# Optimization experiments

Hardware: AMD Instinct MI355X
Metric: run time of the kernel (lower is better)

Reference implementation:

```python
import jax, jax.numpy as jnp
import numpy as np

UNITS = 14336
IN_FEATURES = 4096
PACKED = IN_FEATURES // 4  # 4 ternary values (2 bits each) per byte
CLIP_VAL = 100.0

# 2-bit crumb -> ternary value lookup: 0 -> 0, 1 -> +1, 2 -> -1, 3 -> 0
_TERNARY_LUT = jnp.array([0.0, 1.0, -1.0, 0.0], dtype=jnp.float32)


def _unpack_ternary(pw):
    """pw: [U, P] int (byte values 0..255) -> dense ternary float W [U, 4*P].
    Little-endian crumbs within each byte (shifts 0,2,4,6)."""
    crumbs = jnp.stack([(pw >> (2 * i)) & 3 for i in range(4)], axis=-1)  # [U, P, 4]
    crumbs = crumbs.reshape(pw.shape[0], -1)  # [U, 4*P]
    return _TERNARY_LUT[crumbs][:, :IN_FEATURES]  # [U, IN]


def setup_inputs() -> dict:
    key = jax.random.key(0)
    k1, k2, k3, k4 = jax.random.split(key, 4)
    x = jax.random.normal(k1, (32, IN_FEATURES), dtype=jnp.float32)
    # packed ternary weights, one uint8-valued byte per 4 ternary weights
    pw = jax.random.randint(k2, (UNITS, PACKED), 0, 256, dtype=jnp.int32)
    scale = 1.0 + 0.02 * jax.random.normal(k3, (UNITS,), dtype=jnp.float32)
    bias = 0.01 * jax.random.normal(k4, (UNITS,), dtype=jnp.float32)
    return {"x": x, "pw": pw, "scale": scale, "bias": bias}


def reference(x, pw, scale, bias):
    # dense ternary weight [UNITS, IN]; kernel target would fuse this unpack into the GEMM
    W = _unpack_ternary(pw)
    y = jnp.einsum('bd,ud->bu', x, W)  # [B, UNITS]
    y = y * scale + bias               # per-unit affine dequant
    return jnp.clip(y, -CLIP_VAL, CLIP_VAL)
```

## Files before the change

### kernel.cpp

```cpp
#include <hip/hip_runtime.h>

#define UNITS 14336
#define IN_F 4096
#define PACKED 1024
#define CLIP_VAL 100.0f

typedef unsigned int uint32;

using bf16x8 = __attribute__((ext_vector_type(8))) short;
using f32x4  = __attribute__((ext_vector_type(4))) float;

__device__ uint4 g_xw[16384];

__device__ inline unsigned short f2bf(float f) {
    uint32 u = __float_as_uint(f);
    u += 0x7FFFu + ((u >> 16) & 1u);
    return (unsigned short)(u >> 16);
}

__device__ inline uint32 pack2bf(float a, float b) {
    return (uint32)f2bf(a) | ((uint32)f2bf(b) << 16);
}

__device__ inline void unpack_byte(int v, uint32& r0, uint32& r1) {
    uint32 t0 = ((uint32)v & 3u) | (((uint32)v & 0xCu) << 14);
    uint32 t1 = (((uint32)v >> 4) & 3u) | (((uint32)v & 0xC0u) << 10);
    uint32 s0 = t0 >> 1;
    uint32 s1 = t1 >> 1;
    uint32 nz0 = (t0 ^ s0) & 0x00010001u;
    uint32 nz1 = (t1 ^ s1) & 0x00010001u;
    r0 = nz0 * 0x3F80u + ((s0 & 0x00010001u) << 15);
    r1 = nz1 * 0x3F80u + ((s1 & 0x00010001u) << 15);
}

__device__ inline float clipf(float y) {
    return fminf(fmaxf(y, -CLIP_VAL), CLIP_VAL);
}


__global__ __launch_bounds__(256) void convert_x_kernel(
    const float* __restrict__ x) {
    int t = blockIdx.x * 256 + threadIdx.x;
    int lane = t & 63;
    int h = (t >> 6) & 1;
    int s = (t >> 7) & 1;
    int g = t >> 8;
    int n = lane & 15;
    int q = lane >> 4;
    int b = h * 16 + n;
    int k0 = g * 64 + q * 16 + s * 8;
    const float4* src = (const float4*)(x + (size_t)b * IN_F + k0);
    float4 lo = src[0];
    float4 hi = src[1];
    uint4 o;
    o.x = pack2bf(lo.x, lo.y);
    o.y = pack2bf(lo.z, lo.w);
    o.z = pack2bf(hi.x, hi.y);
    o.w = pack2bf(hi.z, hi.w);
    g_xw[t] = o;
}

__global__ __launch_bounds__(1024, 8) void ternary_mm_kernel(
    const int*   __restrict__ pw,
    const float* __restrict__ scale,
    const float* __restrict__ bias,
    float*       __restrict__ out) {
    __shared__ int lds4[16640];
    char* lds = (char*)lds4;

    const int tid  = threadIdx.x;
    const int wid  = tid >> 6;
    const int lane = tid & 63;
    const int q    = lane >> 4;
    const int n    = lane & 15;
    const int u0   = blockIdx.x << 4;
    const int g0   = wid << 2;

    {
        const char* src = (const char*)(pw + (size_t)u0 * PACKED);
        #pragma unroll
        for (int j = 0; j < 4; ++j) {
            const int Rs = j * 16 + wid;
            __builtin_amdgcn_global_load_lds(
                (const __attribute__((address_space(1))) uint32*)
                    (src + (Rs << 10) + (lane << 4)),
                (__attribute__((address_space(3))) uint32*)
                    (lds + Rs * 1040),
                16, 0, 0);
        }
    }

    const uint4* xb = g_xw + (g0 << 8) + lane;
    uint4 xa0 = xb[0], xa1 = xb[64], xa2 = xb[128], xa3 = xb[192];

    __syncthreads();

    f32x4 acc0 = {0.f,0.f,0.f,0.f};
    f32x4 acc1 = {0.f,0.f,0.f,0.f};

    const int R = (n << 2) + (wid >> 2);
    const char* lb = lds + R * 1040 + ((wid & 3) << 8) + (q << 4);

    #pragma unroll
    for (int i = 0; i < 4; ++i) {
        uint4 xn0, xn1, xn2, xn3;
        if (i < 3) {
            const uint4* xi = xb + ((i + 1) << 8);
            xn0 = xi[0]; xn1 = xi[64]; xn2 = xi[128]; xn3 = xi[192];
        }
        int4 w4 = *(const int4*)(lb + (i << 6));

        uint4 fA, fB;
        unpack_byte(w4.x, fA.x, fA.y);
        unpack_byte(w4.y, fA.z, fA.w);
        unpack_byte(w4.z, fB.x, fB.y);
        unpack_byte(w4.w, fB.z, fB.w);
        bf16x8 vA = __builtin_bit_cast(bf16x8, fA);
        bf16x8 vB = __builtin_bit_cast(bf16x8, fB);

        acc0 = __builtin_amdgcn_mfma_f32_16x16x32_bf16(
            __builtin_bit_cast(bf16x8, xa0), vA, acc0, 0, 0, 0);
        acc1 = __builtin_amdgcn_mfma_f32_16x16x32_bf16(
            __builtin_bit_cast(bf16x8, xa1), vA, acc1, 0, 0, 0);
        acc0 = __builtin_amdgcn_mfma_f32_16x16x32_bf16(
            __builtin_bit_cast(bf16x8, xa2), vB, acc0, 0, 0, 0);
        acc1 = __builtin_amdgcn_mfma_f32_16x16x32_bf16(
            __builtin_bit_cast(bf16x8, xa3), vB, acc1, 0, 0, 0);

        if (i < 3) { xa0 = xn0; xa1 = xn1; xa2 = xn2; xa3 = xn3; }
    }

    __syncthreads();
    f32x4* red = (f32x4*)lds;
    red[(wid * 2 + 0) * 64 + lane] = acc0;
    red[(wid * 2 + 1) * 64 + lane] = acc1;
    __syncthreads();

    if (tid < 128) {
        const int h = tid >> 6;
        const int l = tid & 63;
        f32x4 s = red[h * 64 + l];
        #pragma unroll
        for (int w = 1; w < 16; ++w) {
            f32x4 v = red[(w * 2 + h) * 64 + l];
            s[0] += v[0]; s[1] += v[1]; s[2] += v[2]; s[3] += v[3];
        }
        const int u  = u0 + (l & 15);
        const int b0 = h * 16 + ((l >> 4) << 2);
        const float sc = scale[u];
        const float bi = bias[u];
        float* o = out + (size_t)b0 * UNITS + u;
        o[0 * UNITS] = clipf(s[0] * sc + bi);
        o[1 * UNITS] = clipf(s[1] * sc + bi);
        o[2 * UNITS] = clipf(s[2] * sc + bi);
        o[3 * UNITS] = clipf(s[3] * sc + bi);
    }
}

extern "C" void kernel_launch(void* const* d_in, const int* in_sizes, int n_in,
                              void* d_out, int out_size, void* d_ws, size_t ws_size,
                              hipStream_t stream) {
    const float* x     = (const float*)d_in[0];
    const int*   pw    = (const int*)d_in[1];
    const float* scale = (const float*)d_in[2];
    const float* bias  = (const float*)d_in[3];
    float* out = (float*)d_out;

    (void)d_ws; (void)ws_size;

    convert_x_kernel<<<64, 256, 0, stream>>>(x);
    ternary_mm_kernel<<<UNITS / 16, 1024, 0, stream>>>(pw, scale, bias, out);
}
```

Measured before the change: 103.9 us.

## Fuse x bf16 conversion into ternary GEMM and halve block size

Removes the separate convert_x kernel and its global bf16 staging buffer, so each block now loads fp32 x directly and converts it to bf16 in registers before the MFMAs. The block shrinks from 16 to 8 waves, each covering twice the K range with an 8-iteration loop, and the cross-wave reduction drops to 8 partials. This saves one kernel launch and the round trip through global memory, but every block now reads fp32 x (twice the bytes of bf16) and redoes the conversion, which adds redundant ALU and L2 traffic across all 896 blocks.

```diff
diff --git a/kernel.cpp b/kernel.cpp
--- a/kernel.cpp
+++ b/kernel.cpp
@@ -1,4 +1,5 @@
 #include <hip/hip_runtime.h>
+#include <hip/hip_bf16.h>
 
 #define UNITS 14336
 #define IN_F 4096
@@ -10,16 +11,10 @@
 using bf16x8 = __attribute__((ext_vector_type(8))) short;
 using f32x4  = __attribute__((ext_vector_type(4))) float;
 
-__device__ uint4 g_xw[16384];
-
-__device__ inline unsigned short f2bf(float f) {
-    uint32 u = __float_as_uint(f);
-    u += 0x7FFFu + ((u >> 16) & 1u);
-    return (unsigned short)(u >> 16);
-}
-
 __device__ inline uint32 pack2bf(float a, float b) {
-    return (uint32)f2bf(a) | ((uint32)f2bf(b) << 16);
+    unsigned short lo = __builtin_bit_cast(unsigned short, __float2bfloat16(a));
+    unsigned short hi = __builtin_bit_cast(unsigned short, __float2bfloat16(b));
+    return (uint32)lo | ((uint32)hi << 16);
 }
 
 __device__ inline void unpack_byte(int v, uint32& r0, uint32& r1) {
@@ -37,30 +32,8 @@
     return fminf(fmaxf(y, -CLIP_VAL), CLIP_VAL);
 }
 
-
-__global__ __launch_bounds__(256) void convert_x_kernel(
-    const float* __restrict__ x) {
-    int t = blockIdx.x * 256 + threadIdx.x;
-    int lane = t & 63;
-    int h = (t >> 6) & 1;
-    int s = (t >> 7) & 1;
-    int g = t >> 8;
-    int n = lane & 15;
-    int q = lane >> 4;
-    int b = h * 16 + n;
-    int k0 = g * 64 + q * 16 + s * 8;
-    const float4* src = (const float4*)(x + (size_t)b * IN_F + k0);
-    float4 lo = src[0];
-    float4 hi = src[1];
-    uint4 o;
-    o.x = pack2bf(lo.x, lo.y);
-    o.y = pack2bf(lo.z, lo.w);
-    o.z = pack2bf(hi.x, hi.y);
-    o.w = pack2bf(hi.z, hi.w);
-    g_xw[t] = o;
-}
-
-__global__ __launch_bounds__(1024, 8) void ternary_mm_kernel(
+__global__ __launch_bounds__(512, 4) void ternary_mm_fused(
+    const float* __restrict__ x,
     const int*   __restrict__ pw,
     const float* __restrict__ scale,
     const float* __restrict__ bias,
@@ -74,13 +47,12 @@
     const int q    = lane >> 4;
     const int n    = lane & 15;
     const int u0   = blockIdx.x << 4;
-    const int g0   = wid << 2;
 
     {
         const char* src = (const char*)(pw + (size_t)u0 * PACKED);
         #pragma unroll
-        for (int j = 0; j < 4; ++j) {
-            const int Rs = j * 16 + wid;
+        for (int j = 0; j < 8; ++j) {
+            const int Rs = j * 8 + wid;
             __builtin_amdgcn_global_load_lds(
                 (const __attribute__((address_space(1))) uint32*)
                     (src + (Rs << 10) + (lane << 4)),
@@ -90,24 +62,44 @@
         }
     }
 
-    const uint4* xb = g_xw + (g0 << 8) + lane;
-    uint4 xa0 = xb[0], xa1 = xb[64], xa2 = xb[128], xa3 = xb[192];
+    const float* xp0 = x + (size_t)n * IN_F + (wid << 9) + (q << 4);
+    const float* xp1 = xp0 + (size_t)16 * IN_F;
+
+    float4 a0, a1, a2, a3, b0, b1, b2, b3;
+    {
+        const float4* p0 = (const float4*)xp0;
+        const float4* p1 = (const float4*)xp1;
+        a0 = p0[0]; a1 = p0[1]; a2 = p0[2]; a3 = p0[3];
+        b0 = p1[0]; b1 = p1[1]; b2 = p1[2]; b3 = p1[3];
+    }
 
     __syncthreads();
 
     f32x4 acc0 = {0.f,0.f,0.f,0.f};
     f32x4 acc1 = {0.f,0.f,0.f,0.f};
 
-    const int R = (n << 2) + (wid >> 2);
-    const char* lb = lds + R * 1040 + ((wid & 3) << 8) + (q << 4);
+    const int R = (n << 2) + (wid >> 1);
+    const char* lb = lds + R * 1040 + ((wid & 1) << 9) + (q << 4);
 
     #pragma unroll
-    for (int i = 0; i < 4; ++i) {
-        uint4 xn0, xn1, xn2, xn3;
-        if (i < 3) {
-            const uint4* xi = xb + ((i + 1) << 8);
-            xn0 = xi[0]; xn1 = xi[64]; xn2 = xi[128]; xn3 = xi[192];
+    for (int i = 0; i < 8; ++i) {
+        uint4 xa0, xa1, xa2, xa3;
+        xa0.x = pack2bf(a0.x, a0.y); xa0.y = pack2bf(a0.z, a0.w);
+        xa0.z = pack2bf(a1.x, a1.y); xa0.w = pack2bf(a1.z, a1.w);
+        xa2.x = pack2bf(a2.x, a2.y); xa2.y = pack2bf(a2.z, a2.w);
+        xa2.z = pack2bf(a3.x, a3.y); xa2.w = pack2bf(a3.z, a3.w);
+        xa1.x = pack2bf(b0.x, b0.y); xa1.y = pack2bf(b0.z, b0.w);
+        xa1.z = pack2bf(b1.x, b1.y); xa1.w = pack2bf(b1.z, b1.w);
+        xa3.x = pack2bf(b2.x, b2.y); xa3.y = pack2bf(b2.z, b2.w);
+        xa3.z = pack2bf(b3.x, b3.y); xa3.w = pack2bf(b3.z, b3.w);
+
+        if (i < 7) {
+            const float4* p0 = (const float4*)(xp0 + ((i + 1) << 6));
+            const float4* p1 = (const float4*)(xp1 + ((i + 1) << 6));
+            a0 = p0[0]; a1 = p0[1]; a2 = p0[2]; a3 = p0[3];
+            b0 = p1[0]; b1 = p1[1]; b2 = p1[2]; b3 = p1[3];
         }
+
         int4 w4 = *(const int4*)(lb + (i << 6));
 
         uint4 fA, fB;
@@ -126,8 +118,6 @@
             __builtin_bit_cast(bf16x8, xa2), vB, acc0, 0, 0, 0);
         acc1 = __builtin_amdgcn_mfma_f32_16x16x32_bf16(
             __builtin_bit_cast(bf16x8, xa3), vB, acc1, 0, 0, 0);
-
-        if (i < 3) { xa0 = xn0; xa1 = xn1; xa2 = xn2; xa3 = xn3; }
     }
 
     __syncthreads();
@@ -141,15 +131,15 @@
         const int l = tid & 63;
         f32x4 s = red[h * 64 + l];
         #pragma unroll
-        for (int w = 1; w < 16; ++w) {
+        for (int w = 1; w < 8; ++w) {
             f32x4 v = red[(w * 2 + h) * 64 + l];
             s[0] += v[0]; s[1] += v[1]; s[2] += v[2]; s[3] += v[3];
         }
         const int u  = u0 + (l & 15);
-        const int b0 = h * 16 + ((l >> 4) << 2);
+        const int b0r = h * 16 + ((l >> 4) << 2);
         const float sc = scale[u];
         const float bi = bias[u];
-        float* o = out + (size_t)b0 * UNITS + u;
+        float* o = out + (size_t)b0r * UNITS + u;
         o[0 * UNITS] = clipf(s[0] * sc + bi);
         o[1 * UNITS] = clipf(s[1] * sc + bi);
         o[2 * UNITS] = clipf(s[2] * sc + bi);
@@ -168,6 +158,5 @@
 
     (void)d_ws; (void)ws_size;
 
-    convert_x_kernel<<<64, 256, 0, stream>>>(x);
-    ternary_mm_kernel<<<UNITS / 16, 1024, 0, stream>>>(pw, scale, bias, out);
+    ternary_mm_fused<<<UNITS / 16, 512, 0, stream>>>(x, pw, scale, bias, out);
 }
```

Result: slower. 146.1 us (+40.5%).
